# Kernel tuning notes

Measured on AMD Instinct MI355X. Metric: run time of the kernel, lower is better.

Reference implementation:

```python
import jax, jax.numpy as jnp
from jax import lax
import numpy as np

D_MODEL, D_STATE, D_CONV, D_INNER = 1024, 16, 4, 2048
BATCH, SEQ = 2, 2048


def setup_inputs() -> dict:
    key = jax.random.key(0)
    ks = jax.random.split(key, 7)
    s = lambda fan: 1.0 / np.sqrt(fan)
    return {
        "x": jax.random.normal(ks[0], (BATCH, SEQ, D_MODEL), jnp.float32),
        "W_in": jax.random.normal(ks[1], (2 * D_INNER, D_MODEL), jnp.float32) * s(D_MODEL),
        "conv_w": jax.random.normal(ks[2], (D_INNER, 1, D_CONV), jnp.float32) * s(D_CONV),
        "conv_b": jax.random.normal(ks[3], (D_INNER,), jnp.float32) * 0.02,
        "A_log": jax.random.normal(ks[4], (D_INNER, D_STATE), jnp.float32),
        "W_x": jax.random.normal(ks[5], (2 * D_STATE + 1, D_INNER), jnp.float32) * s(D_INNER),
        "W_out": jax.random.normal(ks[6], (D_MODEL, D_INNER), jnp.float32) * s(D_INNER),
    }


def reference(x, W_in, conv_w, conv_b, A_log, W_x, W_out):
    B, L, _ = x.shape
    di, ds = D_INNER, D_STATE

    # in_proj and chunk into (x_proj, z)
    xz = jnp.einsum("bld,ed->ble", x, W_in)          # [B, L, 2*di]
    xp, z = xz[..., :di], xz[..., di:]

    # depthwise causal conv1d: padding = d_conv-1 on left, then trim to L
    xc = jnp.transpose(xp, (0, 2, 1))                 # [B, di, L]
    xc = lax.conv_general_dilated(
        xc, conv_w, window_strides=(1,), padding=[(D_CONV - 1, 0)],
        feature_group_count=di)
    xc = xc + conv_b[None, :, None]
    xc = jnp.transpose(xc, (0, 2, 1))                 # [B, L, di]
    xc = jax.nn.silu(xc)

    A = -jnp.exp(A_log.astype(jnp.float32))           # [di, ds]

    # input-dependent delta, B, C
    xdbl = jnp.einsum("bld,ed->ble", xc, W_x)         # [B, L, 2*ds+1]
    delta = jax.nn.softplus(xdbl[..., :1])            # [B, L, 1]
    Bm = xdbl[..., 1:1 + ds]                          # [B, L, ds]
    Cm = xdbl[..., 1 + ds:]                           # [B, L, ds]

    # selective scan: h_t = exp(delta_t * A) * h_{t-1} + delta_t * B_t (outer) u_t
    def step(h, inp):
        d_t, b_t, c_t, u_t = inp                      # [B,1], [B,ds], [B,ds], [B,di]
        dA = jnp.exp(d_t[:, :, None] * A[None])       # [B, di, ds]
        h = dA * h + d_t[:, :, None] * b_t[:, None, :] * u_t[:, :, None]
        y_t = jnp.einsum("bds,bs->bd", h, c_t)        # [B, di]
        return h, y_t

    h0 = jnp.zeros((B, di, ds), xc.dtype)
    inps = (jnp.swapaxes(delta, 0, 1), jnp.swapaxes(Bm, 0, 1),
            jnp.swapaxes(Cm, 0, 1), jnp.swapaxes(xc, 0, 1))
    _, ys = lax.scan(step, h0, inps)                  # ys: [L, B, di]
    y = jnp.swapaxes(ys, 0, 1)                        # [B, L, di]

    y = y * jax.nn.silu(z)
    return jnp.einsum("bld,ed->ble", y, W_out)        # [B, L, d_model]
```

## Files before the change

kernel.cpp:

```cpp
#include <hip/hip_runtime.h>

#define DM    1024
#define DS    16
#define DI    2048
#define LSEQ  2048
#define BL    4096
#define NC    64
#define CHK   32

typedef float          f32x4  __attribute__((ext_vector_type(4)));
typedef float          f32x16 __attribute__((ext_vector_type(16)));
typedef unsigned int   u32x4  __attribute__((ext_vector_type(4)));
typedef unsigned short u16x8  __attribute__((ext_vector_type(8)));

__device__ __forceinline__ unsigned short f2bf(float f) {
    unsigned int u = __float_as_uint(f);
    u += 0x7fffu + ((u >> 16) & 1u);
    return (unsigned short)(u >> 16);
}

__device__ __forceinline__ float bf2f(unsigned short u) {
    return __uint_as_float((unsigned int)u << 16);
}

__device__ __forceinline__ float silu_f(float x) {
    return x / (1.f + __expf(-x));
}

__device__ __forceinline__ void mfma_bf16(f32x4& d, const u32x4& a, const u32x4& b) {
    asm("v_mfma_f32_16x16x32_bf16 %0, %1, %2, %0" : "+v"(d) : "v"(a), "v"(b));
}

__device__ __forceinline__ void gload16(const void* g, void* l) {
    __builtin_amdgcn_global_load_lds(
        (const __attribute__((address_space(1))) unsigned int*)g,
        (__attribute__((address_space(3))) unsigned int*)l, 16, 0, 0);
}

__global__ __launch_bounds__(256) void prep_inputs_kernel(const float* __restrict__ x,
                                                          const float* __restrict__ W_in,
                                                          unsigned short* __restrict__ xbf,
                                                          unsigned short* __restrict__ wbf) {
    const int n4 = (BL * DM) / 4;
    int i = blockIdx.x * 256 + threadIdx.x;
    const float* src = (i < n4) ? x : W_in;
    unsigned short* dst = (i < n4) ? xbf : wbf;
    int j = (i < n4) ? i : i - n4;
    float4 v = *(const float4*)(src + j * 4);
    ushort4 o;
    o.x = f2bf(v.x); o.y = f2bf(v.y); o.z = f2bf(v.z); o.w = f2bf(v.w);
    *(ushort4*)(dst + j * 4) = o;
}

__global__ __launch_bounds__(256) void prep_weights_kernel(const float* __restrict__ W_out,
                                                           const float* __restrict__ Wx,
                                                           unsigned short* __restrict__ wobf,
                                                           unsigned short* __restrict__ wxbf) {
    const int n4 = (DM * DI) / 4;
    int i = blockIdx.x * 256 + threadIdx.x;
    if (i < n4) {
        float4 v = *(const float4*)(W_out + i * 4);
        ushort4 o;
        o.x = f2bf(v.x); o.y = f2bf(v.y); o.z = f2bf(v.z); o.w = f2bf(v.w);
        *(ushort4*)(wobf + i * 4) = o;
    } else {
        int j = i - n4;
        if (j < 128 * 2048) {
            int e = j >> 11;
            wxbf[j] = (e < 33) ? f2bf(Wx[j]) : (unsigned short)0;
        }
    }
}

template <typename OUT>
__global__ __launch_bounds__(512, 2) void gemm256_bf16_nt(const unsigned short* __restrict__ A,
                                                          const unsigned short* __restrict__ B,
                                                          OUT* __restrict__ C,
                                                          int M, int N, int K) {
    __shared__ unsigned short As[4][256 * 32];
    __shared__ unsigned short Bs[4][256 * 32];

    const int tid  = threadIdx.x;
    const int lane = tid & 63;
    const int wave = tid >> 6;
    const int wm = wave >> 2;
    const int wn = wave & 3;
    const int lrow = lane & 15, lkh = lane >> 4;
    const int swa  = (lrow >> 1) & 3;

    const long m0 = (long)blockIdx.y * 256;
    const long n0 = (long)blockIdx.x * 256;

    const int scb = ((tid & 3) ^ ((tid >> 3) & 3)) * 8;
    const unsigned short* pa = A + (m0 + (tid >> 2)) * K + scb;
    const unsigned short* pb = B + (n0 + (tid >> 2)) * K + scb;
    const long rstep = (long)128 * K;

    const int NT = K >> 5;

    f32x4 acc[8][4];
#pragma unroll
    for (int i = 0; i < 8; ++i)
#pragma unroll
        for (int j = 0; j < 4; ++j)
            acc[i][j] = (f32x4){0.f, 0.f, 0.f, 0.f};

#define STAGE_A(t) { char* d_ = (char*)&As[(t) & 3][0] + wave * 1024;          \
                     gload16(pa + (long)(t) * 32,         d_);                 \
                     gload16(pa + rstep + (long)(t) * 32, d_ + 8192); }
#define STAGE_B(t) { char* d_ = (char*)&Bs[(t) & 3][0] + wave * 1024;          \
                     gload16(pb + (long)(t) * 32,         d_);                 \
                     gload16(pb + rstep + (long)(t) * 32, d_ + 8192); }

    STAGE_A(0); STAGE_B(0);
    STAGE_A(1); STAGE_B(1);
    STAGE_A(2); STAGE_B(2);
    asm volatile("s_waitcnt vmcnt(8)" ::: "memory");
    __builtin_amdgcn_s_barrier();
    __builtin_amdgcn_sched_barrier(0);

    for (int t = 0; t < NT; ++t) {
        const unsigned short* as = &As[t & 3][0];
        const unsigned short* bs = &Bs[t & 3][0];
        const bool st = (t + 3 < NT);

        u32x4 af[4], bfr[4];
#pragma unroll
        for (int j = 0; j < 4; ++j)
            bfr[j] = *(const u32x4*)(bs + (wn * 64 + j * 16 + lrow) * 32 + ((lkh ^ swa) * 8));
#pragma unroll
        for (int i = 0; i < 4; ++i)
            af[i] = *(const u32x4*)(as + (wm * 128 + i * 16 + lrow) * 32 + ((lkh ^ swa) * 8));
        if (st) STAGE_A(t + 3);
        asm volatile("s_waitcnt lgkmcnt(0)" ::: "memory");
        __builtin_amdgcn_sched_barrier(0);
        __builtin_amdgcn_s_setprio(1);
#pragma unroll
        for (int i = 0; i < 4; ++i)
#pragma unroll
            for (int j = 0; j < 4; ++j)
                mfma_bf16(acc[i][j], af[i], bfr[j]);
        __builtin_amdgcn_s_setprio(0);

#pragma unroll
        for (int i = 0; i < 4; ++i)
            af[i] = *(const u32x4*)(as + (wm * 128 + (i + 4) * 16 + lrow) * 32 + ((lkh ^ swa) * 8));
        if (st) STAGE_B(t + 3);
        asm volatile("s_waitcnt lgkmcnt(0)" ::: "memory");
        __builtin_amdgcn_sched_barrier(0);
        __builtin_amdgcn_s_setprio(1);
#pragma unroll
        for (int i = 0; i < 4; ++i)
#pragma unroll
            for (int j = 0; j < 4; ++j)
                mfma_bf16(acc[i + 4][j], af[i], bfr[j]);
        __builtin_amdgcn_s_setprio(0);

        if (t < NT - 1) {
            if (t <= NT - 4)      asm volatile("s_waitcnt vmcnt(8)" ::: "memory");
            else if (t == NT - 3) asm volatile("s_waitcnt vmcnt(4)" ::: "memory");
            else                  asm volatile("s_waitcnt vmcnt(0)" ::: "memory");
            __builtin_amdgcn_s_barrier();
            __builtin_amdgcn_sched_barrier(0);
        }
    }
#undef STAGE_A
#undef STAGE_B

    asm volatile("s_nop 7\n\ts_nop 7" ::: "memory");

#pragma unroll
    for (int i = 0; i < 8; ++i)
#pragma unroll
        for (int j = 0; j < 4; ++j)
#pragma unroll
            for (int r = 0; r < 4; ++r) {
                long row = m0 + wm * 128 + i * 16 + lkh * 4 + r;
                long col = n0 + wn * 64 + j * 16 + lrow;
                float v = acc[i][j][r];
                if constexpr (sizeof(OUT) == 2) C[row * (long)N + col] = f2bf(v);
                else                            C[row * (long)N + col] = v;
            }
}

template <int NF, typename OUT>
__global__ __launch_bounds__(256) void gemm_bf16_nt(const unsigned short* __restrict__ A,
                                                    const unsigned short* __restrict__ B,
                                                    OUT* __restrict__ C,
                                                    int M, int N, int K, int KS) {
    constexpr int BN = NF * 32;
    __shared__ unsigned short As[2][128 * 32];
    __shared__ unsigned short Bs[2][BN * 32];

    const int tid  = threadIdx.x;
    const int lane = tid & 63;
    const int wave = tid >> 6;
    const int wr = wave >> 1, wc = wave & 1;
    const int lrow = lane & 15, lkh = lane >> 4;

    const long m0 = (long)blockIdx.y * 128;
    const long n0 = (long)blockIdx.x * BN;
    const int koff = blockIdx.z * KS;

    const int scb = ((tid & 3) ^ ((tid >> 3) & 3)) * 8;
    const unsigned short* pa = A + (m0 + (tid >> 2)) * K + koff + scb;
    const unsigned short* pb = B + (n0 + (tid >> 2)) * K + koff + scb;
    const long half = (long)64 * K;

    OUT* Cz = C + (long)blockIdx.z * M * (long)N;

    const int swa = (lrow >> 1) & 3;

    f32x4 acc[4][NF];
#pragma unroll
    for (int i = 0; i < 4; ++i)
#pragma unroll
        for (int j = 0; j < NF; ++j)
            acc[i][j] = (f32x4){0.f, 0.f, 0.f, 0.f};

    auto STAGE = [&](int buf, int k0) {
        char* a = (char*)&As[buf][0] + wave * 1024;
        gload16(pa + k0,        a);
        gload16(pa + half + k0, a + 4096);
        char* b = (char*)&Bs[buf][0] + wave * 1024;
        gload16(pb + k0, b);
        if constexpr (NF == 4) gload16(pb + half + k0, b + 4096);
    };

    STAGE(0, 0);
    asm volatile("s_waitcnt vmcnt(0)" ::: "memory");
    __builtin_amdgcn_s_barrier();
    __builtin_amdgcn_sched_barrier(0);

    int cur = 0;
    for (int k0 = 0; k0 < KS; k0 += 32) {
        const bool notlast = (k0 + 32 < KS);
        if (notlast) STAGE(cur ^ 1, k0 + 32);

        u32x4 af[4], bfr[NF];
#pragma unroll
        for (int i = 0; i < 4; ++i)
            af[i] = *(const u32x4*)(&As[cur][(wr * 64 + i * 16 + lrow) * 32 + ((lkh ^ swa) * 8)]);
#pragma unroll
        for (int j = 0; j < NF; ++j)
            bfr[j] = *(const u32x4*)(&Bs[cur][(wc * NF * 16 + j * 16 + lrow) * 32 + ((lkh ^ swa) * 8)]);

        __builtin_amdgcn_s_setprio(1);
#pragma unroll
        for (int i = 0; i < 4; ++i)
#pragma unroll
            for (int j = 0; j < NF; ++j)
                mfma_bf16(acc[i][j], af[i], bfr[j]);
        __builtin_amdgcn_s_setprio(0);

        if (notlast) {
            asm volatile("s_waitcnt vmcnt(0)" ::: "memory");
            __builtin_amdgcn_s_barrier();
            __builtin_amdgcn_sched_barrier(0);
            cur ^= 1;
        }
    }

    asm volatile("s_nop 7\n\ts_nop 7" ::: "memory");

#pragma unroll
    for (int i = 0; i < 4; ++i)
#pragma unroll
        for (int j = 0; j < NF; ++j)
#pragma unroll
            for (int r = 0; r < 4; ++r) {
                long row = m0 + wr * 64 + i * 16 + lkh * 4 + r;
                long col = n0 + wc * NF * 16 + j * 16 + lrow;
                float v = acc[i][j][r];
                if constexpr (sizeof(OUT) == 2) Cz[row * (long)N + col] = f2bf(v);
                else                            Cz[row * (long)N + col] = v;
            }
}

__global__ __launch_bounds__(256) void conv_silu_kernel(const unsigned short* __restrict__ xzbf,
                                                        const float* __restrict__ cw,
                                                        const float* __restrict__ cb,
                                                        unsigned short* __restrict__ xcbf) {
    int idx = blockIdx.x * 256 + threadIdx.x;
    int d8 = (idx & 255) * 8;
    int m  = idx >> 8;
    int t  = m & (LSEQ - 1);
    const unsigned short* p = xzbf + (long)m * (2 * DI) + d8;
    u16x8 tap0 = (u16x8)(0), tap1 = (u16x8)(0), tap2 = (u16x8)(0);
    u16x8 tap3 = *(const u16x8*)(p);
    if (t >= 1) tap2 = *(const u16x8*)(p - 1 * 2 * DI);
    if (t >= 2) tap1 = *(const u16x8*)(p - 2 * 2 * DI);
    if (t >= 3) tap0 = *(const u16x8*)(p - 3 * 2 * DI);

    u16x8 o;
#pragma unroll
    for (int k = 0; k < 8; ++k) {
        const float4 wv = *(const float4*)(cw + 4 * (d8 + k));
        float s = cb[d8 + k];
        s = fmaf(bf2f(tap0[k]), wv.x, s);
        s = fmaf(bf2f(tap1[k]), wv.y, s);
        s = fmaf(bf2f(tap2[k]), wv.z, s);
        s = fmaf(bf2f(tap3[k]), wv.w, s);
        o[k] = f2bf(silu_f(s));
    }
    *(u16x8*)(xcbf + (long)m * DI + d8) = o;
}

__global__ __launch_bounds__(256) void xdbl_reduce_kernel(const float* __restrict__ part,
                                                          float* __restrict__ dlt,
                                                          float* __restrict__ BC) {
    int idx = blockIdx.x * 256 + threadIdx.x;
    if (idx >= BL * 33) return;
    int m = idx / 33;
    int j = idx - m * 33;
    float v = 0.f;
#pragma unroll
    for (int g = 0; g < 8; ++g) v += part[(long)g * (BL * 128) + (long)m * 128 + j];
    if (j == 0) dlt[m] = (v > 20.f) ? v : log1pf(expf(v));
    else        BC[(long)m * 32 + (j - 1)] = v;
}

__global__ __launch_bounds__(256) void scan_pass1(const float* __restrict__ dlt,
                                                  const float* __restrict__ BC,
                                                  const unsigned short* __restrict__ xcbf,
                                                  const float* __restrict__ A_log,
                                                  float* __restrict__ P_,
                                                  float* __restrict__ S_) {
    __shared__ float sdl[CHK];
    __shared__ float sbc[CHK * 32];

    const int tid = threadIdx.x;
    const int c   = blockIdx.x;
    const int ch  = blockIdx.y * 256 + tid;
    const int b   = ch >> 11;
    const int d   = ch & (DI - 1);
    const long m0 = (long)b * LSEQ + (long)c * CHK;

    *(float4*)(sbc + tid * 4) = *(const float4*)(BC + m0 * 32 + tid * 4);
    if (tid < CHK) sdl[tid] = dlt[m0 + tid];

    f32x16 A, h, P;
#pragma unroll
    for (int s = 0; s < 16; ++s) {
        A[s] = -__expf(A_log[d * 16 + s]);
        h[s] = 0.f;
        P[s] = 1.f;
    }
    const unsigned short* ur = xcbf + m0 * DI + d;
    __syncthreads();

    for (int t = 0; t < CHK; ++t) {
        float dl = sdl[t];
        float u  = bf2f(ur[(long)t * DI]);
        float du = dl * u;
#pragma unroll
        for (int q = 0; q < 4; ++q) {
            f32x4 bq = *(const f32x4*)(sbc + t * 32 + q * 4);
#pragma unroll
            for (int j = 0; j < 4; ++j) {
                const int s = q * 4 + j;
                float dA = __expf(dl * A[s]);
                P[s] *= dA;
                h[s] = fmaf(dA, h[s], du * bq[j]);
            }
        }
    }
    float* pp = P_ + ((long)c * 4096 + ch) * 16;
    float* sp = S_ + ((long)c * 4096 + ch) * 16;
#pragma unroll
    for (int q = 0; q < 4; ++q) {
        *(f32x4*)(pp + q * 4) = (f32x4){P[q*4], P[q*4+1], P[q*4+2], P[q*4+3]};
        *(f32x4*)(sp + q * 4) = (f32x4){h[q*4], h[q*4+1], h[q*4+2], h[q*4+3]};
    }
}

__global__ __launch_bounds__(256) void scan_pass2(const float* __restrict__ P_,
                                                  float* __restrict__ S_) {
    const long idx = (long)blockIdx.x * 256 + threadIdx.x;
    float h = 0.f;
    for (int c0 = 0; c0 < NC; c0 += 8) {
        float p[8], s[8];
#pragma unroll
        for (int i = 0; i < 8; ++i) {
            p[i] = P_[(long)(c0 + i) * 65536 + idx];
            s[i] = S_[(long)(c0 + i) * 65536 + idx];
        }
#pragma unroll
        for (int i = 0; i < 8; ++i) {
            S_[(long)(c0 + i) * 65536 + idx] = h;
            h = fmaf(p[i], h, s[i]);
        }
    }
}

__global__ __launch_bounds__(256) void scan_pass3(const float* __restrict__ dlt,
                                                  const float* __restrict__ BC,
                                                  const unsigned short* __restrict__ xcbf,
                                                  const unsigned short* __restrict__ xzbf,
                                                  const float* __restrict__ A_log,
                                                  const float* __restrict__ H0,
                                                  unsigned short* __restrict__ ybf) {
    __shared__ float sdl[CHK];
    __shared__ float sbc[CHK * 32];

    const int tid = threadIdx.x;
    const int c   = blockIdx.x;
    const int ch  = blockIdx.y * 256 + tid;
    const int b   = ch >> 11;
    const int d   = ch & (DI - 1);
    const long m0 = (long)b * LSEQ + (long)c * CHK;

    *(float4*)(sbc + tid * 4) = *(const float4*)(BC + m0 * 32 + tid * 4);
    if (tid < CHK) sdl[tid] = dlt[m0 + tid];

    f32x16 A, h;
    const float* h0p = H0 + ((long)c * 4096 + ch) * 16;
    {
        f32x4 h0a = *(const f32x4*)(h0p + 0);
        f32x4 h0b = *(const f32x4*)(h0p + 4);
        f32x4 h0c = *(const f32x4*)(h0p + 8);
        f32x4 h0d = *(const f32x4*)(h0p + 12);
#pragma unroll
        for (int j = 0; j < 4; ++j) {
            h[j]      = h0a[j];
            h[4 + j]  = h0b[j];
            h[8 + j]  = h0c[j];
            h[12 + j] = h0d[j];
        }
    }
#pragma unroll
    for (int s = 0; s < 16; ++s) A[s] = -__expf(A_log[d * 16 + s]);

    const unsigned short* ur = xcbf + m0 * DI + d;
    const unsigned short* zr = xzbf + m0 * (2 * DI) + DI + d;
    unsigned short* yr = ybf + m0 * DI + d;
    __syncthreads();

    for (int t = 0; t < CHK; ++t) {
        float dl = sdl[t];
        float u  = bf2f(ur[(long)t * DI]);
        float z  = bf2f(zr[(long)t * 2 * DI]);
        float du = dl * u;
        float y = 0.f;
#pragma unroll
        for (int q = 0; q < 4; ++q) {
            f32x4 bq = *(const f32x4*)(sbc + t * 32 + q * 4);
            f32x4 cq = *(const f32x4*)(sbc + t * 32 + 16 + q * 4);
#pragma unroll
            for (int j = 0; j < 4; ++j) {
                const int s = q * 4 + j;
                float dA = __expf(dl * A[s]);
                h[s] = fmaf(dA, h[s], du * bq[j]);
                y = fmaf(h[s], cq[j], y);
            }
        }
        yr[(long)t * DI] = f2bf(y * silu_f(z));
    }
}

extern "C" void kernel_launch(void* const* d_in, const int* in_sizes, int n_in,
                              void* d_out, int out_size, void* d_ws, size_t ws_size,
                              hipStream_t stream) {
    const float* x      = (const float*)d_in[0];
    const float* W_in   = (const float*)d_in[1];
    const float* conv_w = (const float*)d_in[2];
    const float* conv_b = (const float*)d_in[3];
    const float* A_log  = (const float*)d_in[4];
    const float* W_x    = (const float*)d_in[5];
    const float* W_out  = (const float*)d_in[6];
    float* out = (float*)d_out;

    char* w = (char*)d_ws;
    unsigned short* xbf  = (unsigned short*)(w + 0);
    unsigned short* wbf  = (unsigned short*)(w + 8388608);
    unsigned short* xzbf = (unsigned short*)(w + 16777216);
    unsigned short* xcbf = (unsigned short*)(w + 50331648);
    float*          dlt  = (float*)(w + 67108864);
    float*          BC   = (float*)(w + 67125248);
    float*          P_   = (float*)(w + 67649536);
    float*          S_   = (float*)(w + 84426752);

    unsigned short* wobf      = xbf;
    unsigned short* wxbf      = (unsigned short*)(w + 8388608);
    float*          xdbl_part = (float*)P_;
    unsigned short* ybf       = (unsigned short*)P_;

    prep_inputs_kernel<<<dim3(8192), dim3(256), 0, stream>>>(x, W_in, xbf, wbf);
    gemm256_bf16_nt<unsigned short><<<dim3(16, 16), dim3(512), 0, stream>>>(xbf, wbf, xzbf, BL, 2 * DI, DM);
    prep_weights_kernel<<<dim3(3072), dim3(256), 0, stream>>>(W_out, W_x, wobf, wxbf);
    conv_silu_kernel<<<dim3((BL * DI / 8) / 256), dim3(256), 0, stream>>>(xzbf, conv_w, conv_b, xcbf);
    gemm_bf16_nt<4, float><<<dim3(1, 32, 8), dim3(256), 0, stream>>>(xcbf, wxbf, xdbl_part, BL, 128, DI, 256);
    xdbl_reduce_kernel<<<dim3(528), dim3(256), 0, stream>>>(xdbl_part, dlt, BC);
    scan_pass1<<<dim3(NC, 16), dim3(256), 0, stream>>>(dlt, BC, xcbf, A_log, P_, S_);
    scan_pass2<<<dim3(256), dim3(256), 0, stream>>>(P_, S_);
    scan_pass3<<<dim3(NC, 16), dim3(256), 0, stream>>>(dlt, BC, xcbf, xzbf, A_log, S_, ybf);
    gemm_bf16_nt<2, float><<<dim3(16, 32, 1), dim3(256), 0, stream>>>(ybf, wobf, out, BL, DM, DI, DI);
}
```

Measured before the change: 214.2 us.

## Halve scan chunk size and derive chunk decay from summed delta

```diff
diff --git a/kernel.cpp b/kernel.cpp
--- a/kernel.cpp
+++ b/kernel.cpp
@@ -5,8 +5,8 @@
 #define DI    2048
 #define LSEQ  2048
 #define BL    4096
-#define NC    64
-#define CHK   32
+#define NC    128
+#define CHK   16
 
 typedef float          f32x4  __attribute__((ext_vector_type(4)));
 typedef float          f32x16 __attribute__((ext_vector_type(16)));
@@ -320,12 +320,12 @@
     else        BC[(long)m * 32 + (j - 1)] = v;
 }
 
-__global__ __launch_bounds__(256) void scan_pass1(const float* __restrict__ dlt,
-                                                  const float* __restrict__ BC,
-                                                  const unsigned short* __restrict__ xcbf,
-                                                  const float* __restrict__ A_log,
-                                                  float* __restrict__ P_,
-                                                  float* __restrict__ S_) {
+__global__ __launch_bounds__(256, 4) void scan_pass1(const float* __restrict__ dlt,
+                                                     const float* __restrict__ BC,
+                                                     const unsigned short* __restrict__ xcbf,
+                                                     const float* __restrict__ A_log,
+                                                     float* __restrict__ P_,
+                                                     float* __restrict__ S_) {
     __shared__ float sdl[CHK];
     __shared__ float sbc[CHK * 32];
 
@@ -336,32 +336,42 @@
     const int d   = ch & (DI - 1);
     const long m0 = (long)b * LSEQ + (long)c * CHK;
 
-    *(float4*)(sbc + tid * 4) = *(const float4*)(BC + m0 * 32 + tid * 4);
+    if (tid < CHK * 8) *(float4*)(sbc + tid * 4) = *(const float4*)(BC + m0 * 32 + tid * 4);
     if (tid < CHK) sdl[tid] = dlt[m0 + tid];
 
-    f32x16 A, h, P;
+    f32x16 A2, h;
 #pragma unroll
     for (int s = 0; s < 16; ++s) {
-        A[s] = -__expf(A_log[d * 16 + s]);
+        A2[s] = -__expf(A_log[d * 16 + s]) * 1.44269504f;
         h[s] = 0.f;
-        P[s] = 1.f;
     }
     const unsigned short* ur = xcbf + m0 * DI + d;
+    float sumdl = 0.f;
     __syncthreads();
 
-    for (int t = 0; t < CHK; ++t) {
-        float dl = sdl[t];
-        float u  = bf2f(ur[(long)t * DI]);
-        float du = dl * u;
-#pragma unroll
-        for (int q = 0; q < 4; ++q) {
-            f32x4 bq = *(const f32x4*)(sbc + t * 32 + q * 4);
-#pragma unroll
-            for (int j = 0; j < 4; ++j) {
-                const int s = q * 4 + j;
-                float dA = __expf(dl * A[s]);
-                P[s] *= dA;
-                h[s] = fmaf(dA, h[s], du * bq[j]);
+#pragma unroll
+    for (int t0 = 0; t0 < CHK; t0 += 4) {
+        float uu[4], dd[4];
+#pragma unroll
+        for (int k = 0; k < 4; ++k) {
+            uu[k] = bf2f(ur[(long)(t0 + k) * DI]);
+            dd[k] = sdl[t0 + k];
+        }
+#pragma unroll
+        for (int k = 0; k < 4; ++k) {
+            const int t = t0 + k;
+            float dl = dd[k];
+            float du = dl * uu[k];
+            sumdl += dl;
+#pragma unroll
+            for (int q = 0; q < 4; ++q) {
+                f32x4 bq = *(const f32x4*)(sbc + t * 32 + q * 4);
+#pragma unroll
+                for (int j = 0; j < 4; ++j) {
+                    const int s = q * 4 + j;
+                    float dA = exp2f(dl * A2[s]);
+                    h[s] = fmaf(dA, h[s], du * bq[j]);
+                }
             }
         }
     }
@@ -369,7 +379,10 @@
     float* sp = S_ + ((long)c * 4096 + ch) * 16;
 #pragma unroll
     for (int q = 0; q < 4; ++q) {
-        *(f32x4*)(pp + q * 4) = (f32x4){P[q*4], P[q*4+1], P[q*4+2], P[q*4+3]};
+        f32x4 pv;
+#pragma unroll
+        for (int j = 0; j < 4; ++j) pv[j] = exp2f(A2[q * 4 + j] * sumdl);
+        *(f32x4*)(pp + q * 4) = pv;
         *(f32x4*)(sp + q * 4) = (f32x4){h[q*4], h[q*4+1], h[q*4+2], h[q*4+3]};
     }
 }
@@ -393,13 +406,13 @@
     }
 }
 
-__global__ __launch_bounds__(256) void scan_pass3(const float* __restrict__ dlt,
-                                                  const float* __restrict__ BC,
-                                                  const unsigned short* __restrict__ xcbf,
-                                                  const unsigned short* __restrict__ xzbf,
-                                                  const float* __restrict__ A_log,
-                                                  const float* __restrict__ H0,
-                                                  unsigned short* __restrict__ ybf) {
+__global__ __launch_bounds__(256, 4) void scan_pass3(const float* __restrict__ dlt,
+                                                     const float* __restrict__ BC,
+                                                     const unsigned short* __restrict__ xcbf,
+                                                     const unsigned short* __restrict__ xzbf,
+                                                     const float* __restrict__ A_log,
+                                                     const float* __restrict__ H0,
+                                                     unsigned short* __restrict__ ybf) {
     __shared__ float sdl[CHK];
     __shared__ float sbc[CHK * 32];
 
@@ -410,10 +423,10 @@
     const int d   = ch & (DI - 1);
     const long m0 = (long)b * LSEQ + (long)c * CHK;
 
-    *(float4*)(sbc + tid * 4) = *(const float4*)(BC + m0 * 32 + tid * 4);
+    if (tid < CHK * 8) *(float4*)(sbc + tid * 4) = *(const float4*)(BC + m0 * 32 + tid * 4);
     if (tid < CHK) sdl[tid] = dlt[m0 + tid];
 
-    f32x16 A, h;
+    f32x16 A2, h;
     const float* h0p = H0 + ((long)c * 4096 + ch) * 16;
     {
         f32x4 h0a = *(const f32x4*)(h0p + 0);
@@ -429,32 +442,43 @@
         }
     }
 #pragma unroll
-    for (int s = 0; s < 16; ++s) A[s] = -__expf(A_log[d * 16 + s]);
+    for (int s = 0; s < 16; ++s) A2[s] = -__expf(A_log[d * 16 + s]) * 1.44269504f;
 
     const unsigned short* ur = xcbf + m0 * DI + d;
     const unsigned short* zr = xzbf + m0 * (2 * DI) + DI + d;
     unsigned short* yr = ybf + m0 * DI + d;
     __syncthreads();
 
-    for (int t = 0; t < CHK; ++t) {
-        float dl = sdl[t];
-        float u  = bf2f(ur[(long)t * DI]);
-        float z  = bf2f(zr[(long)t * 2 * DI]);
-        float du = dl * u;
-        float y = 0.f;
-#pragma unroll
-        for (int q = 0; q < 4; ++q) {
-            f32x4 bq = *(const f32x4*)(sbc + t * 32 + q * 4);
-            f32x4 cq = *(const f32x4*)(sbc + t * 32 + 16 + q * 4);
-#pragma unroll
-            for (int j = 0; j < 4; ++j) {
-                const int s = q * 4 + j;
-                float dA = __expf(dl * A[s]);
-                h[s] = fmaf(dA, h[s], du * bq[j]);
-                y = fmaf(h[s], cq[j], y);
+#pragma unroll
+    for (int t0 = 0; t0 < CHK; t0 += 4) {
+        float uu[4], zz[4], dd[4];
+#pragma unroll
+        for (int k = 0; k < 4; ++k) {
+            uu[k] = bf2f(ur[(long)(t0 + k) * DI]);
+            zz[k] = bf2f(zr[(long)(t0 + k) * 2 * DI]);
+            dd[k] = sdl[t0 + k];
+        }
+#pragma unroll
+        for (int k = 0; k < 4; ++k) {
+            const int t = t0 + k;
+            float dl = dd[k];
+            float du = dl * uu[k];
+            f32x4 yv = (f32x4){0.f, 0.f, 0.f, 0.f};
+#pragma unroll
+            for (int q = 0; q < 4; ++q) {
+                f32x4 bq = *(const f32x4*)(sbc + t * 32 + q * 4);
+                f32x4 cq = *(const f32x4*)(sbc + t * 32 + 16 + q * 4);
+#pragma unroll
+                for (int j = 0; j < 4; ++j) {
+                    const int s = q * 4 + j;
+                    float dA = exp2f(dl * A2[s]);
+                    h[s] = fmaf(dA, h[s], du * bq[j]);
+                    yv[q] = fmaf(h[s], cq[j], yv[q]);
+                }
             }
-        }
-        yr[(long)t * DI] = f2bf(y * silu_f(z));
+            float y = (yv[0] + yv[1]) + (yv[2] + yv[3]);
+            yr[(long)t * DI] = f2bf(y * silu_f(zz[k]));
+        }
     }
 }
 
@@ -478,7 +502,7 @@
     float*          dlt  = (float*)(w + 67108864);
     float*          BC   = (float*)(w + 67125248);
     float*          P_   = (float*)(w + 67649536);
-    float*          S_   = (float*)(w + 84426752);
+    float*          S_   = (float*)(w + 101203968);
 
     unsigned short* wobf      = xbf;
     unsigned short* wxbf      = (unsigned short*)(w + 8388608);
```

Result: slower. 229.6 us (+7.2%).
